# Optimization experiments

Measured on AMD Instinct MI355X. Metric: run time of the kernel, lower is better.

## Reference

```python
import jax, jax.numpy as jnp
import numpy as np

F_DIM = 64      # feature_size
N_NODES = 64    # node_num
T_LEN = 24      # seq_len
N_HEADS = 8
BATCH = 16
E = F_DIM * N_NODES          # embed_dim = 4096
HD = E // N_HEADS            # head dim = 512


def setup_inputs() -> dict:
    key = jax.random.key(0)
    ks = jax.random.split(key, 5)
    s = 0.02
    return {
        "x": jax.random.normal(ks[0], (BATCH, F_DIM, T_LEN, N_NODES), jnp.float32),
        "Wqkv": jax.random.normal(ks[1], (3 * E, E), jnp.float32) * s,
        "bqkv": jnp.zeros((3 * E,), jnp.float32),
        "Wo": jax.random.normal(ks[2], (E, E), jnp.float32) * s,
        "bo": jnp.zeros((E,), jnp.float32),
        "Wfc": jax.random.normal(ks[3], (F_DIM, F_DIM), jnp.float32) * s,
        "bfc": jnp.zeros((F_DIM,), jnp.float32),
    }


def reference(x, Wqkv, bqkv, Wo, bo, Wfc, bfc):
    # x: [B, F, T, N]. Teacher-forcing branch of the original forward.
    B, T = x.shape[0], T_LEN
    # tokens: permute(2,0,1,3).reshape(T,B,E) -> E index = f*N + n
    xt = jnp.transpose(x, (2, 0, 1, 3)).reshape(T, B, E)  # [T,B,E]
    # in_proj is per-token, so projecting the full sequence once equals
    # the original's per-prefix projections.
    qkv = xt @ Wqkv.T + bqkv                               # [T,B,3E]
    q, k, v = jnp.split(qkv, 3, axis=-1)
    q = q.reshape(T, B, N_HEADS, HD)
    k = k.reshape(T, B, N_HEADS, HD)
    v = v.reshape(T, B, N_HEADS, HD)
    scores = jnp.einsum('qbhd,kbhd->bhqk', q, k) / np.sqrt(HD).astype(x.dtype)
    # NOTE: the original passes a float tril(ones) mask, which torch ADDS to
    # the scores (adds 1.0 on the lower triangle, 0 above). Reproduce exactly.
    tril_add = jnp.tril(jnp.ones((T, T), x.dtype))
    base = scores + tril_add                               # [B,H,T,T]
    # prefix lengths L = t+1 for steps t = 0..T-2
    L = jnp.arange(1, T)                                   # [T-1]
    keymask = jnp.arange(T)[None, :] < L[:, None]          # [T-1, T]
    masked = jnp.where(keymask[:, None, None, None, :], base[None], -jnp.inf)
    w = jax.nn.softmax(masked, axis=-1)                    # [T-1,B,H,T,T]
    ctx = jnp.einsum('tbhqk,kbhd->tbqhd', w, v).reshape(T - 1, B, T, E)
    out = ctx @ Wo.T + bo                                  # [T-1,B,T,E]
    # adaptive avg pool over the L valid query positions of each prefix
    qm = keymask.astype(out.dtype)                         # q < L
    pooled = jnp.einsum('tbqe,tq->tbe', out, qm) / L[:, None, None].astype(out.dtype)
    # torch: [B,E] -> reshape(B*N, F) -> fc -> relu -> reshape(B, F, 1, N)
    pred = jax.nn.relu(pooled.reshape(T - 1, B * N_NODES, F_DIM) @ Wfc.T + bfc)
    preds = pred.reshape(T - 1, B, F_DIM, N_NODES)         # row-major, same as torch
    first = x[:, :, :1, :]                                 # [B,F,1,N]
    rest = jnp.transpose(preds, (1, 2, 0, 3))              # [B,F,T-1,N]
    return jnp.concatenate([first, rest], axis=2)          # [B,F,T,N]
```

## Files before the change

### kernel.cpp

```cpp
#include <hip/hip_runtime.h>
#include <math.h>

#define F_DIM 64
#define N_NODES 64
#define T_LEN 24
#define N_HEADS 8
#define BATCH 16
#define E_DIM 4096
#define HD 512
#define QKV_N 12288
#define MB 384
#define TS 23
#define MP 368
#define MPAD 384

typedef unsigned short ushort_t;
typedef short bf16x8 __attribute__((ext_vector_type(8)));
typedef float f32x4 __attribute__((ext_vector_type(4)));

__device__ inline ushort_t f2bf(float f) {
    return (ushort_t)((__float_as_uint(f) + 0x8000u) >> 16);
}

__device__ inline void async_load16(const ushort_t* g, ushort_t* lds) {
    __builtin_amdgcn_global_load_lds(
        (const __attribute__((address_space(1))) unsigned int*)g,
        (__attribute__((address_space(3))) unsigned int*)lds,
        16, 0, 0);
}

__global__ void k_transpose(const float* __restrict__ x, ushort_t* __restrict__ xt) {
    int m = blockIdx.x;
    int t = m >> 4, b = m & 15;
    const float* xb = x + (size_t)b * (F_DIM * T_LEN * N_NODES) + (size_t)t * N_NODES;
    ushort_t* row = xt + (size_t)m * E_DIM;
    for (int e = threadIdx.x; e < E_DIM; e += 256) {
        int f = e >> 6, n = e & 63;
        row[e] = f2bf(xb[(size_t)f * (T_LEN * N_NODES) + n]);
    }
}

__global__ __launch_bounds__(256) void k_gemm_mfma(
    const ushort_t* __restrict__ A, const float* __restrict__ B,
    float* __restrict__ P, int N, int K, int kc)
{
    __shared__ __align__(16) ushort_t As[384 * 32];
    __shared__ __align__(16) ushort_t Bs[64 * 32];
    const int tid  = threadIdx.x;
    const int wave = tid >> 6, lane = tid & 63;
    const int lr = lane & 15, lq = lane >> 4;
    const int n0 = blockIdx.x * 64;
    const int kz = blockIdx.z * kc;

    f32x4 acc[6][4];
    #pragma unroll
    for (int i = 0; i < 6; ++i)
        #pragma unroll
        for (int j = 0; j < 4; ++j)
            acc[i][j] = (f32x4){0.f, 0.f, 0.f, 0.f};

    const int rb = lane >> 2, kp = (lane & 3) * 8;
    const ushort_t* gA[6];
    ushort_t* lA[6];
    #pragma unroll
    for (int s = 0; s < 6; ++s) {
        int r = (wave * 6 + s) * 16 + rb;
        gA[s] = A + (size_t)r * K + kp;
        lA[s] = As + (wave * 6 + s) * 512;
    }

    for (int k0 = kz; k0 < kz + kc; k0 += 32) {
        #pragma unroll
        for (int s = 0; s < 6; ++s) async_load16(gA[s] + k0, lA[s]);
        #pragma unroll
        for (int s = 0; s < 2; ++s) {
            int e4  = tid + s * 256;
            int row = e4 >> 3;
            int kq  = (e4 & 7) * 4;
            const float4 v = *(const float4*)(B + (size_t)(n0 + row) * K + k0 + kq);
            unsigned int ux = __float_as_uint(v.x) + 0x8000u;
            unsigned int uy = __float_as_uint(v.y) + 0x8000u;
            unsigned int uz = __float_as_uint(v.z) + 0x8000u;
            unsigned int uw = __float_as_uint(v.w) + 0x8000u;
            unsigned int p0 = __builtin_amdgcn_perm(uy, ux, 0x07060302u);
            unsigned int p1 = __builtin_amdgcn_perm(uw, uz, 0x07060302u);
            *(uint2*)&Bs[row * 32 + kq] = make_uint2(p0, p1);
        }
        __syncthreads();
        bf16x8 af[6], bfr[4];
        #pragma unroll
        for (int i = 0; i < 6; ++i)
            af[i] = *(const bf16x8*)&As[(wave * 96 + i * 16 + lr) * 32 + lq * 8];
        #pragma unroll
        for (int j = 0; j < 4; ++j)
            bfr[j] = *(const bf16x8*)&Bs[(j * 16 + lr) * 32 + lq * 8];
        #pragma unroll
        for (int i = 0; i < 6; ++i)
            #pragma unroll
            for (int j = 0; j < 4; ++j)
                acc[i][j] = __builtin_amdgcn_mfma_f32_16x16x32_bf16(af[i], bfr[j], acc[i][j], 0, 0, 0);
        __syncthreads();
    }

    float* Pz = P + (size_t)blockIdx.z * MPAD * N;
    #pragma unroll
    for (int i = 0; i < 6; ++i) {
        int m = wave * 96 + i * 16 + lq * 4;
        #pragma unroll
        for (int r = 0; r < 4; ++r) {
            #pragma unroll
            for (int j = 0; j < 4; ++j)
                Pz[(size_t)(m + r) * N + n0 + j * 16 + lr] = acc[i][j][r];
        }
    }
}

__global__ void k_reduce(const float* __restrict__ P, const float* __restrict__ bias,
                         float* __restrict__ C, int N, int S) {
    int idx = blockIdx.x * 256 + threadIdx.x;
    size_t e = (size_t)idx * 4;
    int n = (int)(e % N);
    float4 a = *(const float4*)(P + e);
    for (int s = 1; s < S; ++s) {
        const float4 b = *(const float4*)(P + (size_t)s * MPAD * N + e);
        a.x += b.x; a.y += b.y; a.z += b.z; a.w += b.w;
    }
    const float4 bb = *(const float4*)(bias + n);
    a.x += bb.x; a.y += bb.y; a.z += bb.z; a.w += bb.w;
    *(float4*)(C + e) = a;
}

__global__ __launch_bounds__(512) void k_attn(const float* __restrict__ qkv,
                                              ushort_t* __restrict__ cbar) {
    int bh = blockIdx.x;
    int b = bh >> 3, h = bh & 7;
    __shared__ float vs[T_LEN * HD];
    __shared__ float ss[T_LEN][25];
    __shared__ float isv[T_LEN][25];
    __shared__ float wbs[TS * T_LEN];
    int tid = threadIdx.x, wave = tid >> 6, lane = tid & 63;
    for (int i4 = tid; i4 < T_LEN * HD / 4; i4 += 512) {
        int t = i4 >> 7, d4 = (i4 & 127) * 4;
        *(float4*)&vs[t * HD + d4] =
            *(const float4*)&qkv[(size_t)(t * BATCH + b) * QKV_N + 2 * E_DIM + h * HD + d4];
    }
    const float scale = 0.044194173824159216f;
    for (int p = wave; p < T_LEN * T_LEN; p += 8) {
        int qi = p / 24, ki = p - qi * 24;
        const float* qp = qkv + (size_t)(qi * BATCH + b) * QKV_N + h * HD + lane * 8;
        const float* kp = qkv + (size_t)(ki * BATCH + b) * QKV_N + E_DIM + h * HD + lane * 8;
        float4 a0 = *(const float4*)qp, a1 = *(const float4*)(qp + 4);
        float4 c0 = *(const float4*)kp, c1 = *(const float4*)(kp + 4);
        float s = a0.x * c0.x + a0.y * c0.y + a0.z * c0.z + a0.w * c0.w
                + a1.x * c1.x + a1.y * c1.y + a1.z * c1.z + a1.w * c1.w;
        #pragma unroll
        for (int off = 32; off > 0; off >>= 1) s += __shfl_xor(s, off);
        if (lane == 0) {
            s *= scale;
            if (ki <= qi) s += 1.f;
            ss[qi][ki] = s;
        }
    }
    __syncthreads();
    if (tid < T_LEN) {
        int q = tid;
        float M = -1e30f;
        for (int k = 0; k < T_LEN; ++k) M = fmaxf(M, ss[q][k]);
        float run = 0.f;
        for (int k = 0; k < T_LEN; ++k) {
            float e = __expf(ss[q][k] - M);
            ss[q][k] = e;
            run += e;
            isv[q][k] = 1.f / run;
        }
    }
    __syncthreads();
    for (int p = tid; p < TS * T_LEN; p += 512) {
        int t = p / 24, k = p - t * 24;
        float w = 0.f;
        if (k <= t) {
            float sum = 0.f;
            for (int q = 0; q <= t; ++q) sum += ss[q][k] * isv[q][t];
            w = sum / (float)(t + 1);
        }
        wbs[p] = w;
    }
    __syncthreads();
    int d = tid;
    for (int t = 0; t < TS; ++t) {
        float a = 0.f;
        #pragma unroll
        for (int k = 0; k < T_LEN; ++k) a += wbs[t * 24 + k] * vs[k * HD + d];
        cbar[(size_t)(t * BATCH + b) * E_DIM + h * HD + d] = f2bf(a);
    }
}

__global__ void k_final(const float* __restrict__ pooled, const float* __restrict__ Wfc,
                        const float* __restrict__ bfc, float* __restrict__ out) {
    int tb = blockIdx.x;
    int t = tb >> 4, b = tb & 15;
    __shared__ float ps[E_DIM];
    __shared__ float wf[64 * 65];
    __shared__ float bf[64];
    int tid = threadIdx.x;
    for (int i = tid; i < E_DIM; i += 256) ps[i] = pooled[(size_t)tb * E_DIM + i];
    for (int i = tid; i < 64 * 64; i += 256) wf[(i >> 6) * 65 + (i & 63)] = Wfc[i];
    if (tid < 64) bf[tid] = bfc[tid];
    __syncthreads();
    for (int p = tid; p < 4096; p += 256) {
        int f = p >> 6, n = p & 63;
        float acc = bf[n];
        #pragma unroll
        for (int g = 0; g < 64; ++g) acc += ps[f * 64 + g] * wf[n * 65 + g];
        out[(size_t)((b * 64 + f) * T_LEN + (t + 1)) * N_NODES + n] = fmaxf(acc, 0.f);
    }
}

__global__ void k_first(const float* __restrict__ x, float* __restrict__ out) {
    int idx = blockIdx.x * 256 + threadIdx.x;
    if (idx >= BATCH * F_DIM * N_NODES) return;
    int b = idx >> 12, f = (idx >> 6) & 63, n = idx & 63;
    size_t o = ((size_t)(b * 64 + f) * T_LEN) * 64 + n;
    out[o] = x[o];
}

extern "C" void kernel_launch(void* const* d_in, const int* in_sizes, int n_in,
                              void* d_out, int out_size, void* d_ws, size_t ws_size,
                              hipStream_t stream) {
    const float* x    = (const float*)d_in[0];
    const float* Wqkv = (const float*)d_in[1];
    const float* bqkv = (const float*)d_in[2];
    const float* Wo   = (const float*)d_in[3];
    const float* bo   = (const float*)d_in[4];
    const float* Wfc  = (const float*)d_in[5];
    const float* bfc  = (const float*)d_in[6];
    float* out = (float*)d_out;

    char* wsb = (char*)d_ws;
    ushort_t* xt   = (ushort_t*)wsb;
    float*    qkv  = (float*)(wsb + 3145728);
    ushort_t* cbar = (ushort_t*)(wsb + 3145728 + 18874368);
    float*  pooled = (float*)(wsb + 3145728 + 18874368 + 3145728);
    size_t base    = 3145728 + 18874368 + 3145728 + 6291456;
    float*  pbuf   = (float*)(wsb + base);

    const size_t pq = (size_t)MPAD * QKV_N * 4;
    const size_t po = (size_t)MPAD * E_DIM * 4;
    int S = (ws_size >= base + 2 * pq) ? 2 : 1;
    int Swo = (ws_size >= base + 8 * po) ? 8 : ((ws_size >= base + 4 * po) ? 4 : 1);

    hipLaunchKernelGGL(k_transpose, dim3(MB), dim3(256), 0, stream, x, xt);

    hipLaunchKernelGGL(k_gemm_mfma, dim3(QKV_N / 64, 1, S), dim3(256), 0, stream,
                       xt, Wqkv, pbuf, QKV_N, E_DIM, E_DIM / S);
    hipLaunchKernelGGL(k_reduce, dim3(MPAD * QKV_N / 4 / 256), dim3(256), 0, stream,
                       pbuf, bqkv, qkv, QKV_N, S);

    hipLaunchKernelGGL(k_attn, dim3(BATCH * N_HEADS), dim3(512), 0, stream, qkv, cbar);

    hipLaunchKernelGGL(k_gemm_mfma, dim3(E_DIM / 64, 1, Swo), dim3(256), 0, stream,
                       cbar, Wo, pbuf, E_DIM, E_DIM, E_DIM / Swo);
    hipLaunchKernelGGL(k_reduce, dim3(MPAD * E_DIM / 4 / 256), dim3(256), 0, stream,
                       pbuf, bo, pooled, E_DIM, Swo);

    hipLaunchKernelGGL(k_final, dim3(TS * BATCH), dim3(256), 0, stream, pooled, Wfc, bfc, out);
    hipLaunchKernelGGL(k_first, dim3((BATCH * F_DIM * N_NODES + 255) / 256), dim3(256), 0, stream, x, out);
}
```

Before: 539.6 us.

## Fuse split-K reductions into attention and final kernels, raise split-K factors

Removes the two standalone split-K reduction kernels. The partial-sum accumulation and bias add now happen inside the attention kernel (Q/K staged to LDS as bf16, V summed on the fly) and inside the final fc kernel. Split-K factors rise to 8 and 16 when the workspace allows, and the input transpose is vectorised with float4 loads. This saves launches and the round trip of the full qkv/pooled buffers, but the attention kernel re-reads up to S partial buffers with only 128 blocks. Q/K are also rounded to bf16 before the score dot products.

Result: slower. 724.3 us (+34.2%).

```diff
diff --git a/kernel.cpp b/kernel.cpp
--- a/kernel.cpp
+++ b/kernel.cpp
@@ -29,14 +29,23 @@
         16, 0, 0);
 }
 
+__device__ inline float bdot2(unsigned int a, unsigned int c) {
+    float a0 = __uint_as_float(a << 16), a1 = __uint_as_float(a & 0xFFFF0000u);
+    float c0 = __uint_as_float(c << 16), c1 = __uint_as_float(c & 0xFFFF0000u);
+    return a0 * c0 + a1 * c1;
+}
+
 __global__ void k_transpose(const float* __restrict__ x, ushort_t* __restrict__ xt) {
     int m = blockIdx.x;
     int t = m >> 4, b = m & 15;
     const float* xb = x + (size_t)b * (F_DIM * T_LEN * N_NODES) + (size_t)t * N_NODES;
     ushort_t* row = xt + (size_t)m * E_DIM;
-    for (int e = threadIdx.x; e < E_DIM; e += 256) {
+    for (int e4 = threadIdx.x; e4 < E_DIM / 4; e4 += 256) {
+        int e = e4 * 4;
         int f = e >> 6, n = e & 63;
-        row[e] = f2bf(xb[(size_t)f * (T_LEN * N_NODES) + n]);
+        const float4 v = *(const float4*)&xb[(size_t)f * (T_LEN * N_NODES) + n];
+        ushort_t o[4] = {f2bf(v.x), f2bf(v.y), f2bf(v.z), f2bf(v.w)};
+        *(uint2*)&row[e] = *(uint2*)o;
     }
 }
 
@@ -115,44 +124,39 @@
     }
 }
 
-__global__ void k_reduce(const float* __restrict__ P, const float* __restrict__ bias,
-                         float* __restrict__ C, int N, int S) {
-    int idx = blockIdx.x * 256 + threadIdx.x;
-    size_t e = (size_t)idx * 4;
-    int n = (int)(e % N);
-    float4 a = *(const float4*)(P + e);
-    for (int s = 1; s < S; ++s) {
-        const float4 b = *(const float4*)(P + (size_t)s * MPAD * N + e);
-        a.x += b.x; a.y += b.y; a.z += b.z; a.w += b.w;
-    }
-    const float4 bb = *(const float4*)(bias + n);
-    a.x += bb.x; a.y += bb.y; a.z += bb.z; a.w += bb.w;
-    *(float4*)(C + e) = a;
-}
-
-__global__ __launch_bounds__(512) void k_attn(const float* __restrict__ qkv,
-                                              ushort_t* __restrict__ cbar) {
+__global__ __launch_bounds__(512) void k_attn(const float* __restrict__ P,
+                                              const float* __restrict__ bqkv,
+                                              ushort_t* __restrict__ cbar, int S) {
     int bh = blockIdx.x;
     int b = bh >> 3, h = bh & 7;
-    __shared__ float vs[T_LEN * HD];
+    __shared__ __align__(16) ushort_t qs[T_LEN * HD];
+    __shared__ __align__(16) ushort_t ks[T_LEN * HD];
     __shared__ float ss[T_LEN][25];
     __shared__ float isv[T_LEN][25];
-    __shared__ float wbs[TS * T_LEN];
+    __shared__ float wbs[TS][T_LEN];
     int tid = threadIdx.x, wave = tid >> 6, lane = tid & 63;
-    for (int i4 = tid; i4 < T_LEN * HD / 4; i4 += 512) {
-        int t = i4 >> 7, d4 = (i4 & 127) * 4;
-        *(float4*)&vs[t * HD + d4] =
-            *(const float4*)&qkv[(size_t)(t * BATCH + b) * QKV_N + 2 * E_DIM + h * HD + d4];
-    }
+    const size_t pstride = (size_t)MPAD * QKV_N;
+
+    for (int i = tid; i < T_LEN * HD; i += 512) {
+        int t = i >> 9, d = i & 511;
+        size_t rq = (size_t)(t * BATCH + b) * QKV_N + h * HD + d;
+        float q = bqkv[h * HD + d], k = bqkv[E_DIM + h * HD + d];
+        for (int s = 0; s < S; ++s) {
+            q += P[s * pstride + rq];
+            k += P[s * pstride + rq + E_DIM];
+        }
+        qs[i] = f2bf(q);
+        ks[i] = f2bf(k);
+    }
+    __syncthreads();
+
     const float scale = 0.044194173824159216f;
     for (int p = wave; p < T_LEN * T_LEN; p += 8) {
         int qi = p / 24, ki = p - qi * 24;
-        const float* qp = qkv + (size_t)(qi * BATCH + b) * QKV_N + h * HD + lane * 8;
-        const float* kp = qkv + (size_t)(ki * BATCH + b) * QKV_N + E_DIM + h * HD + lane * 8;
-        float4 a0 = *(const float4*)qp, a1 = *(const float4*)(qp + 4);
-        float4 c0 = *(const float4*)kp, c1 = *(const float4*)(kp + 4);
-        float s = a0.x * c0.x + a0.y * c0.y + a0.z * c0.z + a0.w * c0.w
-                + a1.x * c1.x + a1.y * c1.y + a1.z * c1.z + a1.w * c1.w;
+        uint4 qv = *(const uint4*)&qs[qi * HD + lane * 8];
+        uint4 kv = *(const uint4*)&ks[ki * HD + lane * 8];
+        float s = bdot2(qv.x, kv.x) + bdot2(qv.y, kv.y)
+                + bdot2(qv.z, kv.z) + bdot2(qv.w, kv.w);
         #pragma unroll
         for (int off = 32; off > 0; off >>= 1) s += __shfl_xor(s, off);
         if (lane == 0) {
@@ -183,27 +187,42 @@
             for (int q = 0; q <= t; ++q) sum += ss[q][k] * isv[q][t];
             w = sum / (float)(t + 1);
         }
-        wbs[p] = w;
-    }
-    __syncthreads();
+        wbs[t][k] = w;
+    }
+    __syncthreads();
+
     int d = tid;
-    for (int t = 0; t < TS; ++t) {
-        float a = 0.f;
-        #pragma unroll
-        for (int k = 0; k < T_LEN; ++k) a += wbs[t * 24 + k] * vs[k * HD + d];
-        cbar[(size_t)(t * BATCH + b) * E_DIM + h * HD + d] = f2bf(a);
-    }
-}
-
-__global__ void k_final(const float* __restrict__ pooled, const float* __restrict__ Wfc,
-                        const float* __restrict__ bfc, float* __restrict__ out) {
+    float acc[TS];
+    #pragma unroll
+    for (int t = 0; t < TS; ++t) acc[t] = 0.f;
+    const float bv = bqkv[2 * E_DIM + h * HD + d];
+    for (int k = 0; k < T_LEN; ++k) {
+        size_t rv = (size_t)(k * BATCH + b) * QKV_N + 2 * E_DIM + h * HD + d;
+        float v = bv;
+        for (int s = 0; s < S; ++s) v += P[s * pstride + rv];
+        #pragma unroll
+        for (int t = 0; t < TS; ++t) acc[t] += wbs[t][k] * v;
+    }
+    #pragma unroll
+    for (int t = 0; t < TS; ++t)
+        cbar[(size_t)(t * BATCH + b) * E_DIM + h * HD + d] = f2bf(acc[t]);
+}
+
+__global__ void k_final(const float* __restrict__ P, const float* __restrict__ bo,
+                        const float* __restrict__ Wfc, const float* __restrict__ bfc,
+                        float* __restrict__ out, int S) {
     int tb = blockIdx.x;
     int t = tb >> 4, b = tb & 15;
     __shared__ float ps[E_DIM];
     __shared__ float wf[64 * 65];
     __shared__ float bf[64];
     int tid = threadIdx.x;
-    for (int i = tid; i < E_DIM; i += 256) ps[i] = pooled[(size_t)tb * E_DIM + i];
+    const size_t pstride = (size_t)MPAD * E_DIM;
+    for (int i = tid; i < E_DIM; i += 256) {
+        float v = bo[i];
+        for (int s = 0; s < S; ++s) v += P[s * pstride + (size_t)tb * E_DIM + i];
+        ps[i] = v;
+    }
     for (int i = tid; i < 64 * 64; i += 256) wf[(i >> 6) * 65 + (i & 63)] = Wfc[i];
     if (tid < 64) bf[tid] = bfc[tid];
     __syncthreads();
@@ -238,31 +257,34 @@
 
     char* wsb = (char*)d_ws;
     ushort_t* xt   = (ushort_t*)wsb;
-    float*    qkv  = (float*)(wsb + 3145728);
-    ushort_t* cbar = (ushort_t*)(wsb + 3145728 + 18874368);
-    float*  pooled = (float*)(wsb + 3145728 + 18874368 + 3145728);
-    size_t base    = 3145728 + 18874368 + 3145728 + 6291456;
+    ushort_t* cbar = (ushort_t*)(wsb + 3145728);
+    size_t base    = 6291456;
     float*  pbuf   = (float*)(wsb + base);
 
     const size_t pq = (size_t)MPAD * QKV_N * 4;
     const size_t po = (size_t)MPAD * E_DIM * 4;
-    int S = (ws_size >= base + 2 * pq) ? 2 : 1;
-    int Swo = (ws_size >= base + 8 * po) ? 8 : ((ws_size >= base + 4 * po) ? 4 : 1);
+    int S = 1;
+    if      (ws_size >= base + 8 * pq) S = 8;
+    else if (ws_size >= base + 4 * pq) S = 4;
+    else if (ws_size >= base + 2 * pq) S = 2;
+    int Swo = 1;
+    if      (ws_size >= base + 16 * po) Swo = 16;
+    else if (ws_size >= base + 8 * po)  Swo = 8;
+    else if (ws_size >= base + 4 * po)  Swo = 4;
 
     hipLaunchKernelGGL(k_transpose, dim3(MB), dim3(256), 0, stream, x, xt);
 
     hipLaunchKernelGGL(k_gemm_mfma, dim3(QKV_N / 64, 1, S), dim3(256), 0, stream,
                        xt, Wqkv, pbuf, QKV_N, E_DIM, E_DIM / S);
-    hipLaunchKernelGGL(k_reduce, dim3(MPAD * QKV_N / 4 / 256), dim3(256), 0, stream,
-                       pbuf, bqkv, qkv, QKV_N, S);
-
-    hipLaunchKernelGGL(k_attn, dim3(BATCH * N_HEADS), dim3(512), 0, stream, qkv, cbar);
+
+    hipLaunchKernelGGL(k_attn, dim3(BATCH * N_HEADS), dim3(512), 0, stream,
+                       pbuf, bqkv, cbar, S);
 
     hipLaunchKernelGGL(k_gemm_mfma, dim3(E_DIM / 64, 1, Swo), dim3(256), 0, stream,
                        cbar, Wo, pbuf, E_DIM, E_DIM, E_DIM / Swo);
-    hipLaunchKernelGGL(k_reduce, dim3(MPAD * E_DIM / 4 / 256), dim3(256), 0, stream,
-                       pbuf, bo, pooled, E_DIM, Swo);
-
-    hipLaunchKernelGGL(k_final, dim3(TS * BATCH), dim3(256), 0, stream, pooled, Wfc, bfc, out);
+
+    hipLaunchKernelGGL(k_final, dim3(TS * BATCH), dim3(256), 0, stream,
+                       pbuf, bo, Wfc, bfc, out, Swo);
+
     hipLaunchKernelGGL(k_first, dim3((BATCH * F_DIM * N_NODES + 255) / 256), dim3(256), 0, stream, x, out);
 }
```
